# Performance work log

Hardware: AMD Instinct MI355X
Metric: run time of the kernel (lower is better)

The kernel has to match this reference:

```python
import jax, jax.numpy as jnp
import numpy as np

N_TOK = 384
VOCAB = 50000
N_POS = 52
WDIM = 512
HDIM = 1024
FEAT_DIM = 3 * 16  # np.repeat([len,start,end],16)


def setup_inputs() -> dict:
    key = jax.random.key(0)
    ks = jax.random.split(key, 10)
    s = 0.02  # init scale
    return {
        "sentence": jax.random.randint(ks[0], (N_TOK,), 0, VOCAB),
        "pos_tags": jax.random.randint(ks[1], (N_TOK,), 0, N_POS),
        "We_wrd": jax.random.normal(ks[2], (VOCAB, WDIM), jnp.float32) * s,
        "We_pos": jax.random.normal(ks[3], (N_POS, WDIM), jnp.float32) * s,
        "W_dan1": jax.random.normal(ks[4], (2 * WDIM, HDIM), jnp.float32) * s,
        "b_dan1": jnp.zeros((HDIM,), jnp.float32),
        "W_dan2": jax.random.normal(ks[5], (HDIM, HDIM), jnp.float32) * s,
        "b_dan2": jnp.zeros((HDIM,), jnp.float32),
        "W_s1": jax.random.normal(ks[6], (HDIM + FEAT_DIM, HDIM), jnp.float32) * s,
        "b_s1": jnp.zeros((HDIM,), jnp.float32),
        "W_s2": jax.random.normal(ks[7], (HDIM, 1), jnp.float32) * s,
        "b_s2": jnp.zeros((1,), jnp.float32),
    }


def reference(sentence, pos_tags, We_wrd, We_pos, W_dan1, b_dan1, W_dan2, b_dan2, W_s1, b_s1, W_s2, b_s2):
    n = sentence.shape[0]
    # per-token embedding: concat(pos, word) as in score() with use_pos=True -> [n, 2*wdim]
    emb = jnp.concatenate([We_pos[pos_tags], We_wrd[sentence]], axis=-1)
    # prefix sums so every span mean is O(1): pref[k] = sum of emb[:k]
    pref = jnp.concatenate([jnp.zeros((1, emb.shape[1]), emb.dtype), jnp.cumsum(emb, axis=0)], axis=0)
    # all spans (i, j) with i <= j, as in the double loop over i..n-1, j..n-1
    i_idx, j_idx = np.triu_indices(n)  # static shapes, S = n(n+1)/2
    i_idx = jnp.asarray(i_idx)
    j_idx = jnp.asarray(j_idx)
    end = j_idx + 1
    length = (end - i_idx).astype(emb.dtype)
    # DAN encoder: mean of span embeddings -> 2 relu layers (config['layer']=2)
    mean = (pref[end] - pref[i_idx]) / length[:, None]            # [S, 2*wdim]
    h = jax.nn.relu(mean @ W_dan1 + b_dan1)                        # [S, hdim]
    h = jax.nn.relu(h @ W_dan2 + b_dan2)                           # [S, hdim]
    # phrase feats: np.repeat([len, start, end], 16) -> [S, 48]
    feats = jnp.repeat(jnp.stack([length, i_idx.astype(emb.dtype), end.astype(emb.dtype)], axis=1), 16, axis=1)
    rep = jnp.concatenate([h, feats], axis=1)                      # [S, hdim+48]
    # Wpscore MLP: Linear(ph_dim+48 -> hdim) + relu, Linear(hdim -> 1)
    h2 = jax.nn.relu(rep @ W_s1 + b_s1)
    scores = (h2 @ W_s2 + b_s2)[:, 0]                              # [S]
    return scores
```

## Files before the change

### kernel.cpp

```cpp
#include <hip/hip_runtime.h>

#define NTOK  384
#define SPANS 73920
#define MTILES 584
#define MPAD  (MTILES * 128)
#define HD    1024
#define BK    32
#define KTS   (HD / BK)

typedef unsigned short u16;
typedef __attribute__((ext_vector_type(8))) short short8;
typedef __attribute__((ext_vector_type(4))) float floatx4;

#define VMCNT_IMM(N) (((N) & 0xF) | (((N) >> 4) << 14) | (0x7 << 4) | (0xF << 8))

__device__ __forceinline__ u16 f2bu(float x) {
  union { float f; unsigned u; } un; un.f = x;
  unsigned r = un.u + 0x7fffu + ((un.u >> 16) & 1u);
  return (u16)(r >> 16);
}

__device__ __forceinline__ void gld_lds16(const void* g, void* l) {
  __builtin_amdgcn_global_load_lds(
      (const __attribute__((address_space(1))) void*)g,
      (__attribute__((address_space(3))) void*)l, 16, 0, 0);
}

__global__ void emb_gather(const int* __restrict__ sent, const int* __restrict__ pos,
                           const float* __restrict__ Wwrd, const float* __restrict__ Wpos,
                           u16* __restrict__ embB) {
  int t = blockIdx.x;
  int c = threadIdx.x;
  int pt = pos[t], st = sent[t];
  #pragma unroll
  for (int u = 0; u < 4; ++u) {
    int col = u * 256 + c;
    float v = (col < 512) ? Wpos[(size_t)pt * 512 + col]
                          : Wwrd[(size_t)st * 512 + (col - 512)];
    embB[(size_t)t * HD + col] = f2bu(v);
  }
}

__global__ void prep_spans(int* __restrict__ spI, int* __restrict__ spE, float* __restrict__ spInv,
                           float* __restrict__ scores, const float* __restrict__ bs2) {
  int rf = blockIdx.x * 256 + threadIdx.x;
  if (rf >= MPAD) return;
  int s = rf < SPANS ? rf : SPANS - 1;
  const int n = NTOK;
  double tn = 2.0 * n + 1.0;
  int i = (int)((tn - sqrt(tn * tn - 8.0 * (double)s)) * 0.5);
  if (i < 0) i = 0;
  if (i > n - 1) i = n - 1;
  #define OFF(ii) (((ii) * (2 * n - (ii) + 1)) / 2)
  while (i + 1 <= n - 1 && OFF(i + 1) <= s) ++i;
  while (i > 0 && OFF(i) > s) --i;
  int j = i + (s - OFF(i));
  #undef OFF
  spI[rf] = i;
  spE[rf] = j + 1;
  spInv[rf] = 1.0f / (float)(j + 1 - i);
  if (rf < SPANS) scores[rf] = bs2[0];
}

__global__ void prep_castT(const float* __restrict__ Wd1, const float* __restrict__ Wd2,
                           const float* __restrict__ Ws1,
                           u16* __restrict__ o1, u16* __restrict__ o2, u16* __restrict__ o3) {
  int b = blockIdx.x;
  int w = b >> 10, rem = b & 1023;
  int tk = rem >> 5, tn = rem & 31;
  const float* src = (w == 0) ? Wd1 : ((w == 1) ? Wd2 : Ws1);
  u16* dst = (w == 0) ? o1 : ((w == 1) ? o2 : o3);
  __shared__ u16 tile[32][33];
  int x = threadIdx.x & 31, y = threadIdx.x >> 5;
  int k0 = tk * 32, n0 = tn * 32;
  for (int yy = 0; yy < 32; yy += 8)
    tile[y + yy][x] = f2bu(src[(size_t)(k0 + y + yy) * HD + n0 + x]);
  __syncthreads();
  for (int yy = 0; yy < 32; yy += 8)
    dst[(size_t)(n0 + y + yy) * HD + k0 + x] = tile[x][y + yy];
}

__global__ void prep_svec(const float* __restrict__ Ws1,
                          float* __restrict__ S0, float* __restrict__ S1v, float* __restrict__ S2v) {
  int c = blockIdx.x * 256 + threadIdx.x;
  if (c >= HD) return;
  float a = 0.f, b = 0.f, d = 0.f;
  for (int r = 0; r < 16; ++r) {
    a += Ws1[(size_t)(1024 + r) * HD + c];
    b += Ws1[(size_t)(1040 + r) * HD + c];
    d += Ws1[(size_t)(1056 + r) * HD + c];
  }
  S0[c] = a; S1v[c] = b; S2v[c] = d;
}

__global__ void yscan(const float* __restrict__ Y, float* __restrict__ Qp) {
  __shared__ float buf[NTOK];
  int c = blockIdx.x;
  int t = threadIdx.x;
  buf[t] = Y[(size_t)t * HD + c];
  __syncthreads();
  #pragma unroll
  for (int off = 1; off < NTOK; off <<= 1) {
    float add = (t >= off) ? buf[t - off] : 0.f;
    __syncthreads();
    buf[t] += add;
    __syncthreads();
  }
  if (t == 0) Qp[c] = 0.f;
  Qp[(size_t)(t + 1) * HD + c] = buf[t];
}

__global__ void expand(const float* __restrict__ Qp, const int* __restrict__ spI,
                       const int* __restrict__ spE, const float* __restrict__ spInv,
                       const float* __restrict__ b1, u16* __restrict__ out) {
  int gid = blockIdx.x * 256 + threadIdx.x;
  int row = gid >> 7;
  int c0 = (gid & 127) << 3;
  int i = spI[row], e = spE[row];
  float inv = spInv[row];
  const float* pe = Qp + (size_t)e * HD + c0;
  const float* pi = Qp + (size_t)i * HD + c0;
  const float* bb = b1 + c0;
  u16 tmp[8];
  #pragma unroll
  for (int u = 0; u < 8; ++u) {
    float v = (pe[u] - pi[u]) * inv + bb[u];
    v = v > 0.f ? v : 0.f;
    tmp[u] = f2bu(v);
  }
  *(uint4*)(out + (size_t)row * HD + c0) = *(const uint4*)tmp;
}

template <int EPI>
__global__ __launch_bounds__(256, 3) void gemm_bt(
    const u16* __restrict__ A, const u16* __restrict__ Bt,
    const float* __restrict__ bias, u16* __restrict__ C, float* __restrict__ Cf,
    const int* __restrict__ spI, const int* __restrict__ spE,
    const float* __restrict__ S0, const float* __restrict__ S1v, const float* __restrict__ S2v,
    const float* __restrict__ Ws2, float* __restrict__ scores) {
  __shared__ u16 As[2][128 * BK];
  __shared__ u16 Bs[2][128 * BK];
  int bx = blockIdx.x;
  int mt, nt;
  if (EPI == 2) {
    nt = bx & 7; mt = bx >> 3;
  } else {
    int xcd = bx & 7, k = bx >> 3;
    nt = k & 7;
    mt = xcd + 8 * (k >> 3);
  }
  int m0 = mt * 128, n0 = nt * 128;
  int t = threadIdx.x, lane = t & 63, wid = t >> 6;
  int wm = wid >> 1, wn = wid & 1;
  int q = lane >> 4, r = lane & 15;

  floatx4 acc[4][4] = {};

  int dsub = (lane & 7) ^ ((lane >> 3) & 7);
  int row0 = wid * 16 + 2 * (lane >> 3) + (dsub >> 2);
  int voff = row0 * HD + (dsub & 3) * 8;
  const u16* gA0 = A  + (size_t)m0 * HD;
  const u16* gB0 = Bt + (size_t)n0 * HD;
  int ldsOff0 = wid * 512;
  int ldsOff1 = 2048 + wid * 512;

  auto stage = [&](int kt, int b) {
    const u16* pa = gA0 + voff + kt * BK;
    const u16* pb = gB0 + voff + kt * BK;
    gld_lds16(pa,                   &As[b][ldsOff0]);
    gld_lds16(pa + (size_t)64 * HD, &As[b][ldsOff1]);
    gld_lds16(pb,                   &Bs[b][ldsOff0]);
    gld_lds16(pb + (size_t)64 * HD, &Bs[b][ldsOff1]);
  };

  int oct = (((r & 1) << 2) + q) ^ ((r >> 1) & 7);
  int aoff[4], boff[4];
  #pragma unroll
  for (int x = 0; x < 4; ++x) {
    aoff[x] = (wm * 32 + x * 8 + (r >> 1)) * 64 + oct * 8;
    boff[x] = (wn * 32 + x * 8 + (r >> 1)) * 64 + oct * 8;
  }

  auto compute = [&](int b) {
    short8 af[4];
    #pragma unroll
    for (int x = 0; x < 4; ++x) af[x] = *(const short8*)(&As[b][aoff[x]]);
    #pragma unroll
    for (int ni = 0; ni < 4; ++ni) {
      short8 bf = *(const short8*)(&Bs[b][boff[ni]]);
      #pragma unroll
      for (int mi = 0; mi < 4; ++mi)
        acc[mi][ni] = __builtin_amdgcn_mfma_f32_16x16x32_bf16(af[mi], bf, acc[mi][ni], 0, 0, 0);
    }
  };

  stage(0, 0);
  #pragma unroll 1
  for (int kt = 0; kt < KTS; ++kt) {
    int cur = kt & 1;
    if (kt < KTS - 1) {
      stage(kt + 1, cur ^ 1);
      __builtin_amdgcn_s_waitcnt(VMCNT_IMM(4));
    } else {
      __builtin_amdgcn_s_waitcnt(VMCNT_IMM(0));
    }
    __builtin_amdgcn_s_barrier();
    compute(cur);
    __builtin_amdgcn_s_barrier();
  }

  if (EPI == 2) {
    #pragma unroll
    for (int mi = 0; mi < 4; ++mi) {
      int rowb = m0 + wm * 64 + mi * 16 + q * 4;
      #pragma unroll
      for (int ni = 0; ni < 4; ++ni) {
        int col = n0 + wn * 64 + ni * 16 + r;
        #pragma unroll
        for (int e = 0; e < 4; ++e)
          Cf[(size_t)(rowb + e) * HD + col] = acc[mi][ni][e];
      }
    }
  } else if (EPI == 0) {
    #pragma unroll
    for (int mi = 0; mi < 4; ++mi) {
      int rowb = m0 + wm * 64 + mi * 16 + q * 4;
      #pragma unroll
      for (int ni = 0; ni < 4; ++ni) {
        int col = n0 + wn * 64 + ni * 16 + r;
        float bcol = bias[col];
        #pragma unroll
        for (int e = 0; e < 4; ++e) {
          float v = acc[mi][ni][e] + bcol;
          v = v > 0.f ? v : 0.f;
          C[(size_t)(rowb + e) * HD + col] = f2bu(v);
        }
      }
    }
  } else {
    float bcol[4], s0c[4], s1c[4], s2c[4], wsc[4];
    #pragma unroll
    for (int ni = 0; ni < 4; ++ni) {
      int col = n0 + wn * 64 + ni * 16 + r;
      bcol[ni] = bias[col]; s0c[ni] = S0[col]; s1c[ni] = S1v[col];
      s2c[ni] = S2v[col];  wsc[ni] = Ws2[col];
    }
    #pragma unroll
    for (int mi = 0; mi < 4; ++mi) {
      int rowb = m0 + wm * 64 + mi * 16 + q * 4;
      #pragma unroll
      for (int e = 0; e < 4; ++e) {
        int row = rowb + e;
        float fi = (float)spI[row];
        float fe = (float)spE[row];
        float fl = fe - fi;
        float p = 0.f;
        #pragma unroll
        for (int ni = 0; ni < 4; ++ni) {
          float v = acc[mi][ni][e] + bcol[ni] + fl * s0c[ni] + fi * s1c[ni] + fe * s2c[ni];
          v = v > 0.f ? v : 0.f;
          p += v * wsc[ni];
        }
        p += __shfl_xor(p, 1);
        p += __shfl_xor(p, 2);
        p += __shfl_xor(p, 4);
        p += __shfl_xor(p, 8);
        if (r == 0 && row < SPANS) atomicAdd(&scores[row], p);
      }
    }
  }
}

extern "C" void kernel_launch(void* const* d_in, const int* in_sizes, int n_in,
                              void* d_out, int out_size, void* d_ws, size_t ws_size,
                              hipStream_t stream) {
  const int*   sent = (const int*)d_in[0];
  const int*   pos  = (const int*)d_in[1];
  const float* Wwrd = (const float*)d_in[2];
  const float* Wpos = (const float*)d_in[3];
  const float* Wd1  = (const float*)d_in[4];
  const float* bd1  = (const float*)d_in[5];
  const float* Wd2  = (const float*)d_in[6];
  const float* bd2  = (const float*)d_in[7];
  const float* Ws1  = (const float*)d_in[8];
  const float* bs1  = (const float*)d_in[9];
  const float* Ws2  = (const float*)d_in[10];
  const float* bs2  = (const float*)d_in[11];
  float* scores = (float*)d_out;

  char* w = (char*)d_ws;
  size_t o = 0;
  auto alloc = [&](size_t bytes) {
    char* p = w + o;
    o = (o + bytes + 255) & ~(size_t)255;
    return p;
  };
  int*   spI   = (int*)  alloc((size_t)MPAD * 4);
  int*   spE   = (int*)  alloc((size_t)MPAD * 4);
  float* spInv = (float*)alloc((size_t)MPAD * 4);
  float* S0    = (float*)alloc(4096);
  float* S1v   = (float*)alloc(4096);
  float* S2v   = (float*)alloc(4096);
  u16*   embB  = (u16*)  alloc((size_t)NTOK * HD * 2);
  float* Ybuf  = (float*)alloc((size_t)NTOK * HD * 4);
  float* Qp    = (float*)alloc((size_t)(NTOK + 1) * HD * 4);
  u16* Wd1t = (u16*)alloc((size_t)HD * HD * 2);
  u16* Wd2t = (u16*)alloc((size_t)HD * HD * 2);
  u16* Ws1t = (u16*)alloc((size_t)HD * HD * 2);
  u16* bufA = (u16*)alloc((size_t)MPAD * HD * 2);
  u16* bufB = (u16*)alloc((size_t)MPAD * HD * 2);

  emb_gather<<<NTOK, 256, 0, stream>>>(sent, pos, Wwrd, Wpos, embB);
  prep_spans<<<(MPAD + 255) / 256, 256, 0, stream>>>(spI, spE, spInv, scores, bs2);
  prep_castT<<<3 * 1024, 256, 0, stream>>>(Wd1, Wd2, Ws1, Wd1t, Wd2t, Ws1t);
  prep_svec <<<4, 256, 0, stream>>>(Ws1, S0, S1v, S2v);

  gemm_bt<2><<<(NTOK / 128) * 8, 256, 0, stream>>>(embB, Wd1t, nullptr, nullptr, Ybuf,
                                                   nullptr, nullptr, nullptr, nullptr, nullptr,
                                                   nullptr, nullptr);
  yscan<<<HD, NTOK, 0, stream>>>(Ybuf, Qp);
  expand<<<MPAD / 2, 256, 0, stream>>>(Qp, spI, spE, spInv, bd1, bufA);

  gemm_bt<0><<<MTILES * 8, 256, 0, stream>>>(bufA, Wd2t, bd2, bufB, nullptr,
                                             nullptr, nullptr, nullptr, nullptr, nullptr,
                                             nullptr, nullptr);
  gemm_bt<1><<<MTILES * 8, 256, 0, stream>>>(bufB, Ws1t, bs1, nullptr, nullptr,
                                             spI, spE, S0, S1v, S2v, Ws2, scores);
}
```

Measured before the change: 595.2 us.

## Fuse span-mean expansion into second GEMM's A-tile loader and fold bias into prefix

Removes the separate expand kernel and its large bf16 intermediate buffer. The DAN2 GEMM now builds each A tile itself: it gathers prefix-sum rows from Qp, computes the difference times the inverse length, applies ReLU, packs to bf16 and stores into LDS. The first-layer bias moves into the scan as (t+1)*b, so the prefix difference already contains it. The cost is that A loads become synchronous register loads with ALU work inside the K loop instead of async global-to-LDS copies, and each tile reads fp32 gathered data.

```diff
diff --git a/kernel.cpp b/kernel.cpp
--- a/kernel.cpp
+++ b/kernel.cpp
@@ -1,4 +1,5 @@
 #include <hip/hip_runtime.h>
+#include <hip/hip_bf16.h>
 
 #define NTOK  384
 #define SPANS 73920
@@ -12,12 +13,19 @@
 typedef __attribute__((ext_vector_type(8))) short short8;
 typedef __attribute__((ext_vector_type(4))) float floatx4;
 
-#define VMCNT_IMM(N) (((N) & 0xF) | (((N) >> 4) << 14) | (0x7 << 4) | (0xF << 8))
+#define VM_IMM(N)      (((N) & 0xF) | (((N) >> 4) << 14) | (0x7 << 4) | (0xF << 8))
+#define VM_LGKM0(N)    (((N) & 0xF) | (((N) >> 4) << 14) | (0x7 << 4) | (0x0 << 8))
 
 __device__ __forceinline__ u16 f2bu(float x) {
   union { float f; unsigned u; } un; un.f = x;
   unsigned r = un.u + 0x7fffu + ((un.u >> 16) & 1u);
   return (u16)(r >> 16);
+}
+
+__device__ __forceinline__ unsigned pk2(float a, float b) {
+  union { __hip_bfloat162 h; unsigned u; } un;
+  un.h = __float22bfloat162_rn(float2{a, b});
+  return un.u;
 }
 
 __device__ __forceinline__ void gld_lds16(const void* g, void* l) {
@@ -93,7 +101,8 @@
   S0[c] = a; S1v[c] = b; S2v[c] = d;
 }
 
-__global__ void yscan(const float* __restrict__ Y, float* __restrict__ Qp) {
+__global__ void yscan(const float* __restrict__ Y, float* __restrict__ Qp,
+                      const float* __restrict__ b1) {
   __shared__ float buf[NTOK];
   int c = blockIdx.x;
   int t = threadIdx.x;
@@ -106,36 +115,17 @@
     buf[t] += add;
     __syncthreads();
   }
+  float bc = b1[c];
   if (t == 0) Qp[c] = 0.f;
-  Qp[(size_t)(t + 1) * HD + c] = buf[t];
-}
-
-__global__ void expand(const float* __restrict__ Qp, const int* __restrict__ spI,
-                       const int* __restrict__ spE, const float* __restrict__ spInv,
-                       const float* __restrict__ b1, u16* __restrict__ out) {
-  int gid = blockIdx.x * 256 + threadIdx.x;
-  int row = gid >> 7;
-  int c0 = (gid & 127) << 3;
-  int i = spI[row], e = spE[row];
-  float inv = spInv[row];
-  const float* pe = Qp + (size_t)e * HD + c0;
-  const float* pi = Qp + (size_t)i * HD + c0;
-  const float* bb = b1 + c0;
-  u16 tmp[8];
-  #pragma unroll
-  for (int u = 0; u < 8; ++u) {
-    float v = (pe[u] - pi[u]) * inv + bb[u];
-    v = v > 0.f ? v : 0.f;
-    tmp[u] = f2bu(v);
-  }
-  *(uint4*)(out + (size_t)row * HD + c0) = *(const uint4*)tmp;
-}
-
-template <int EPI>
+  Qp[(size_t)(t + 1) * HD + c] = buf[t] + (float)(t + 1) * bc;
+}
+
+template <int EPI, int ASRC>
 __global__ __launch_bounds__(256, 3) void gemm_bt(
     const u16* __restrict__ A, const u16* __restrict__ Bt,
     const float* __restrict__ bias, u16* __restrict__ C, float* __restrict__ Cf,
-    const int* __restrict__ spI, const int* __restrict__ spE,
+    const float* __restrict__ Qp,
+    const int* __restrict__ spI, const int* __restrict__ spE, const float* __restrict__ spInv,
     const float* __restrict__ S0, const float* __restrict__ S1v, const float* __restrict__ S2v,
     const float* __restrict__ Ws2, float* __restrict__ scores) {
   __shared__ u16 As[2][128 * BK];
@@ -164,13 +154,43 @@
   int ldsOff0 = wid * 512;
   int ldsOff1 = 2048 + wid * 512;
 
+  const float *pe0, *pi0, *pe1, *pi1;
+  float inv0, inv1;
+  if (ASRC == 1) {
+    int g0 = m0 + row0, g1 = g0 + 64;
+    int cofs = (dsub & 3) * 8;
+    pe0 = Qp + (size_t)spE[g0] * HD + cofs;  pi0 = Qp + (size_t)spI[g0] * HD + cofs;
+    pe1 = Qp + (size_t)spE[g1] * HD + cofs;  pi1 = Qp + (size_t)spI[g1] * HD + cofs;
+    inv0 = spInv[g0]; inv1 = spInv[g1];
+  }
+
   auto stage = [&](int kt, int b) {
-    const u16* pa = gA0 + voff + kt * BK;
     const u16* pb = gB0 + voff + kt * BK;
-    gld_lds16(pa,                   &As[b][ldsOff0]);
-    gld_lds16(pa + (size_t)64 * HD, &As[b][ldsOff1]);
     gld_lds16(pb,                   &Bs[b][ldsOff0]);
     gld_lds16(pb + (size_t)64 * HD, &Bs[b][ldsOff1]);
+    if (ASRC == 0) {
+      const u16* pa = gA0 + voff + kt * BK;
+      gld_lds16(pa,                   &As[b][ldsOff0]);
+      gld_lds16(pa + (size_t)64 * HD, &As[b][ldsOff1]);
+    } else {
+      int cb = kt * BK;
+      float4 x0 = *(const float4*)(pe0 + cb), x1 = *(const float4*)(pe0 + cb + 4);
+      float4 y0 = *(const float4*)(pi0 + cb), y1 = *(const float4*)(pi0 + cb + 4);
+      float4 u0 = *(const float4*)(pe1 + cb), u1 = *(const float4*)(pe1 + cb + 4);
+      float4 v0 = *(const float4*)(pi1 + cb), v1 = *(const float4*)(pi1 + cb + 4);
+      float a0 = fmaxf((x0.x - y0.x) * inv0, 0.f), a1 = fmaxf((x0.y - y0.y) * inv0, 0.f);
+      float a2 = fmaxf((x0.z - y0.z) * inv0, 0.f), a3 = fmaxf((x0.w - y0.w) * inv0, 0.f);
+      float a4 = fmaxf((x1.x - y1.x) * inv0, 0.f), a5 = fmaxf((x1.y - y1.y) * inv0, 0.f);
+      float a6 = fmaxf((x1.z - y1.z) * inv0, 0.f), a7 = fmaxf((x1.w - y1.w) * inv0, 0.f);
+      uint4 w0 = {pk2(a0, a1), pk2(a2, a3), pk2(a4, a5), pk2(a6, a7)};
+      *(uint4*)(&As[b][ldsOff0 + lane * 8]) = w0;
+      float b0 = fmaxf((u0.x - v0.x) * inv1, 0.f), b1v = fmaxf((u0.y - v0.y) * inv1, 0.f);
+      float b2 = fmaxf((u0.z - v0.z) * inv1, 0.f), b3 = fmaxf((u0.w - v0.w) * inv1, 0.f);
+      float b4 = fmaxf((u1.x - v1.x) * inv1, 0.f), b5 = fmaxf((u1.y - v1.y) * inv1, 0.f);
+      float b6 = fmaxf((u1.z - v1.z) * inv1, 0.f), b7 = fmaxf((u1.w - v1.w) * inv1, 0.f);
+      uint4 w1 = {pk2(b0, b1v), pk2(b2, b3), pk2(b4, b5), pk2(b6, b7)};
+      *(uint4*)(&As[b][ldsOff1 + lane * 8]) = w1;
+    }
   };
 
   int oct = (((r & 1) << 2) + q) ^ ((r >> 1) & 7);
@@ -194,20 +214,24 @@
     }
   };
 
+  const int NSTG = (ASRC == 0) ? 4 : 2;
   stage(0, 0);
   #pragma unroll 1
   for (int kt = 0; kt < KTS; ++kt) {
     int cur = kt & 1;
     if (kt < KTS - 1) {
       stage(kt + 1, cur ^ 1);
-      __builtin_amdgcn_s_waitcnt(VMCNT_IMM(4));
+      if (ASRC == 0) __builtin_amdgcn_s_waitcnt(VM_IMM(4));
+      else           __builtin_amdgcn_s_waitcnt(VM_LGKM0(2));
     } else {
-      __builtin_amdgcn_s_waitcnt(VMCNT_IMM(0));
+      if (ASRC == 0) __builtin_amdgcn_s_waitcnt(VM_IMM(0));
+      else           __builtin_amdgcn_s_waitcnt(VM_LGKM0(0));
     }
     __builtin_amdgcn_s_barrier();
     compute(cur);
     __builtin_amdgcn_s_barrier();
   }
+  (void)NSTG;
 
   if (EPI == 2) {
     #pragma unroll
@@ -307,7 +331,6 @@
   u16* Wd1t = (u16*)alloc((size_t)HD * HD * 2);
   u16* Wd2t = (u16*)alloc((size_t)HD * HD * 2);
   u16* Ws1t = (u16*)alloc((size_t)HD * HD * 2);
-  u16* bufA = (u16*)alloc((size_t)MPAD * HD * 2);
   u16* bufB = (u16*)alloc((size_t)MPAD * HD * 2);
 
   emb_gather<<<NTOK, 256, 0, stream>>>(sent, pos, Wwrd, Wpos, embB);
@@ -315,15 +338,15 @@
   prep_castT<<<3 * 1024, 256, 0, stream>>>(Wd1, Wd2, Ws1, Wd1t, Wd2t, Ws1t);
   prep_svec <<<4, 256, 0, stream>>>(Ws1, S0, S1v, S2v);
 
-  gemm_bt<2><<<(NTOK / 128) * 8, 256, 0, stream>>>(embB, Wd1t, nullptr, nullptr, Ybuf,
-                                                   nullptr, nullptr, nullptr, nullptr, nullptr,
-                                                   nullptr, nullptr);
-  yscan<<<HD, NTOK, 0, stream>>>(Ybuf, Qp);
-  expand<<<MPAD / 2, 256, 0, stream>>>(Qp, spI, spE, spInv, bd1, bufA);
-
-  gemm_bt<0><<<MTILES * 8, 256, 0, stream>>>(bufA, Wd2t, bd2, bufB, nullptr,
-                                             nullptr, nullptr, nullptr, nullptr, nullptr,
-                                             nullptr, nullptr);
-  gemm_bt<1><<<MTILES * 8, 256, 0, stream>>>(bufB, Ws1t, bs1, nullptr, nullptr,
-                                             spI, spE, S0, S1v, S2v, Ws2, scores);
-}
+  gemm_bt<2, 0><<<(NTOK / 128) * 8, 256, 0, stream>>>(embB, Wd1t, nullptr, nullptr, Ybuf,
+                                                      nullptr, nullptr, nullptr, nullptr,
+                                                      nullptr, nullptr, nullptr, nullptr, nullptr);
+  yscan<<<HD, NTOK, 0, stream>>>(Ybuf, Qp, bd1);
+
+  gemm_bt<0, 1><<<MTILES * 8, 256, 0, stream>>>(nullptr, Wd2t, bd2, bufB, nullptr,
+                                                Qp, spI, spE, spInv,
+                                                nullptr, nullptr, nullptr, nullptr, nullptr);
+  gemm_bt<1, 0><<<MTILES * 8, 256, 0, stream>>>(bufB, Ws1t, bs1, nullptr, nullptr,
+                                                nullptr, spI, spE, spInv,
+                                                S0, S1v, S2v, Ws2, scores);
+}
```

Measured after the change: 597.8 us. No clear change (+0.4%).
